# Kernel tuning notes

Hardware: AMD Instinct MI355X
Metric: run time of the kernel (lower is better)

Reference implementation:

```python
import jax, jax.numpy as jnp
import numpy as np

D_MODEL = 1024
NUM_HEADS = 16
D_HEAD = D_MODEL // NUM_HEADS


def setup_inputs() -> dict:
    key = jax.random.key(0)
    ks = jax.random.split(key, 10)
    B, L = 2, 2048
    s = 1.0 / np.sqrt(D_MODEL)
    inp = {
        'x_q': jax.random.normal(ks[0], (B, L, D_MODEL), jnp.float32),
        'x_kv': jax.random.normal(ks[1], (B, L, D_MODEL), jnp.float32),
        'wq': jax.random.normal(ks[2], (D_MODEL, D_MODEL), jnp.float32) * s,
        'bq': jnp.zeros((D_MODEL,), jnp.float32),
        'wk': jax.random.normal(ks[3], (D_MODEL, D_MODEL), jnp.float32) * s,
        'bk': jnp.zeros((D_MODEL,), jnp.float32),
        'wv': jax.random.normal(ks[4], (D_MODEL, D_MODEL), jnp.float32) * s,
        'bv': jnp.zeros((D_MODEL,), jnp.float32),
        'wo': jax.random.normal(ks[5], (D_MODEL, D_MODEL), jnp.float32) * s,
        'bo': jnp.zeros((D_MODEL,), jnp.float32),
    }
    return inp


def _split_heads(x):
    B, L, _ = x.shape
    return x.reshape(B, L, NUM_HEADS, D_HEAD).transpose(0, 2, 1, 3)  # (B,H,L,Dh)


def reference(x_q, x_kv, wq, bq, wk, bk, wv, bv, wo, bo):
    # Linear projections (torch Linear: x @ W^T + b)
    q = _split_heads(x_q @ wq.T + bq)   # (B,H,Lq,Dh)
    k = _split_heads(x_kv @ wk.T + bk)  # (B,H,Lk,Dh)
    v = _split_heads(x_kv @ wv.T + bv)  # (B,H,Lk,Dh)
    scale = 1.0 / jnp.sqrt(jnp.asarray(D_HEAD, q.dtype))
    scores = jnp.einsum('bhqd,bhkd->bhqk', q, k) * scale
    attn = jax.nn.softmax(scores, axis=-1)
    out = jnp.einsum('bhqk,bhkd->bhqd', attn, v)  # (B,H,Lq,Dh)
    B, H, Lq, Dh = out.shape
    out = out.transpose(0, 2, 1, 3).reshape(B, Lq, H * Dh)
    # dropout is identity in eval mode
    return out @ wo.T + bo
```

## Files before the change

kernel.cpp:

```cpp
#include <hip/hip_runtime.h>
#include <hip/hip_bf16.h>

typedef _Float16 __attribute__((ext_vector_type(8))) half8;
typedef _Float16 __attribute__((ext_vector_type(4))) half4;
typedef __fp16 __attribute__((ext_vector_type(2))) fp16x2;
typedef __fp16 __attribute__((ext_vector_type(4))) fp16x4;
typedef float __attribute__((ext_vector_type(4))) f32x4;

typedef __attribute__((address_space(1))) void gvoid_t;
typedef __attribute__((address_space(3))) void lvoid_t;

__device__ __forceinline__ void gld_lds16(const void* g, void* l) {
    __builtin_amdgcn_global_load_lds((const gvoid_t*)g, (lvoid_t*)l, 16, 0, 0);
}

__global__ void cvt_all(const float* __restrict__ x_q, const float* __restrict__ x_kv,
                        const float* __restrict__ wq, const float* __restrict__ wk,
                        const float* __restrict__ wv, const float* __restrict__ wo,
                        _Float16* __restrict__ xq16, _Float16* __restrict__ xkv16,
                        _Float16* __restrict__ wq16, _Float16* __restrict__ wk16,
                        _Float16* __restrict__ wv16, _Float16* __restrict__ wo16)
{
    const int y = blockIdx.y;
    const int n = (y < 2) ? (4096 * 1024) : (1024 * 1024);
    int i = (blockIdx.x * 256 + threadIdx.x) * 8;
    if (i >= n) return;
    const float* in = (y == 0) ? x_q : (y == 1) ? x_kv : (y == 2) ? wq : (y == 3) ? wk : (y == 4) ? wv : wo;
    _Float16* out = (y == 0) ? xq16 : (y == 1) ? xkv16 : (y == 2) ? wq16 : (y == 3) ? wk16 : (y == 4) ? wv16 : wo16;
    float4 a = *(const float4*)(in + i);
    float4 b = *(const float4*)(in + i + 4);
    half8 h;
    h[0] = (_Float16)a.x; h[1] = (_Float16)a.y; h[2] = (_Float16)a.z; h[3] = (_Float16)a.w;
    h[4] = (_Float16)b.x; h[5] = (_Float16)b.y; h[6] = (_Float16)b.z; h[7] = (_Float16)b.w;
    *(half8*)(out + i) = h;
}

template <typename OutT, bool VT>
__device__ __forceinline__ void gemm_store(
    OutT* __restrict__ C, int N, int row0, int col, float bb, float osc, const f32x4& acc)
{
    if (VT) {
        int b = row0 >> 11, l0 = row0 & 2047, h = col >> 6, dh = col & 63;
        half4 hv;
#pragma unroll
        for (int r = 0; r < 4; ++r) hv[r] = (_Float16)((acc[r] + bb) * osc);
        *(half4*)&C[(size_t)(((b * 16 + h) * 64 + dh)) * 2048 + l0] = hv;
    } else {
#pragma unroll
        for (int r = 0; r < 4; ++r) {
            float v = (acc[r] + bb) * osc;
            C[(size_t)(row0 + r) * N + col] = (OutT)v;
        }
    }
}

template <typename OutT, bool VT>
__device__ __forceinline__ void gemm_body(
    const _Float16* __restrict__ A,
    const _Float16* __restrict__ W,
    const float* __restrict__ bias,
    OutT* __restrict__ C,
    int N, int K, int bm, int bn, float osc,
    _Float16* As, _Float16* Bs)
{
    const int tid = threadIdx.x;
    const int wv = tid >> 6;
    const int lane = tid & 63;
    const int lr = lane & 15;
    const int lk = lane >> 4;
    const int wm = wv >> 1, wn = wv & 1;

    auto stage = [&](int cb, int k0) {
#pragma unroll
        for (int i = 0; i < 2; ++i) {
            int chunk = i * 256 + tid;
            int row = chunk >> 3, c8 = chunk & 7;
            gld_lds16(A + (size_t)(bm * 64 + row) * K + k0 + c8 * 8, &As[cb * 4096 + chunk * 8]);
        }
#pragma unroll
        for (int i = 0; i < 4; ++i) {
            int chunk = i * 256 + tid;
            int row = chunk >> 3, c8 = chunk & 7;
            gld_lds16(W + (size_t)(bn * 128 + row) * K + k0 + c8 * 8, &Bs[cb * 8192 + chunk * 8]);
        }
    };

    f32x4 acc[2][4] = {};

    stage(0, 0);
    __syncthreads();

    for (int k2 = 0; k2 < K; k2 += 128) {
#pragma unroll
        for (int hf = 0; hf < 2; ++hf) {
            const int k0 = k2 + hf * 64;
            if (k0 + 64 < K) stage(hf ^ 1, k0 + 64);
#pragma unroll
            for (int kk = 0; kk < 2; ++kk) {
                half8 a[2], b[4];
#pragma unroll
                for (int m = 0; m < 2; ++m)
                    a[m] = *(const half8*)&As[hf * 4096 + (wm * 32 + m * 16 + lr) * 64 + kk * 32 + lk * 8];
#pragma unroll
                for (int n = 0; n < 4; ++n)
                    b[n] = *(const half8*)&Bs[hf * 8192 + (wn * 64 + n * 16 + lr) * 64 + kk * 32 + lk * 8];
#pragma unroll
                for (int m = 0; m < 2; ++m)
#pragma unroll
                    for (int n = 0; n < 4; ++n)
                        acc[m][n] = __builtin_amdgcn_mfma_f32_16x16x32_f16(a[m], b[n], acc[m][n], 0, 0, 0);
            }
            __syncthreads();
        }
    }

#pragma unroll
    for (int m = 0; m < 2; ++m)
#pragma unroll
        for (int n = 0; n < 4; ++n) {
            int row0 = bm * 64 + wm * 32 + m * 16 + lk * 4;
            int col  = bn * 128 + wn * 64 + n * 16 + lr;
            gemm_store<OutT, VT>(C, N, row0, col, bias[col], osc, acc[m][n]);
        }
}

__device__ __forceinline__ int xcd_swz512(int x) { return ((x & 7) << 6) | (x >> 3); }

template <typename OutT>
__global__ __launch_bounds__(256) void gemm_bt(
    const _Float16* __restrict__ A, const _Float16* __restrict__ W,
    const float* __restrict__ bias, OutT* __restrict__ C,
    int M, int N, int K)
{
    __shared__ _Float16 As[2 * 64 * 64];
    __shared__ _Float16 Bs[2 * 128 * 64];
    const int nbn = N >> 7;
    const int bid = xcd_swz512(blockIdx.x);
    gemm_body<OutT, false>(A, W, bias, C, N, K, bid / nbn, bid % nbn, 1.0f, As, Bs);
}

__global__ __launch_bounds__(256) void gemm_qkv(
    const _Float16* __restrict__ xq, const _Float16* __restrict__ xkv,
    const _Float16* __restrict__ wqp, const _Float16* __restrict__ wkp, const _Float16* __restrict__ wvp,
    const float* __restrict__ bq, const float* __restrict__ bk, const float* __restrict__ bvv,
    _Float16* __restrict__ Qb, _Float16* __restrict__ Kb, _Float16* __restrict__ VbT)
{
    __shared__ _Float16 As[2 * 64 * 64];
    __shared__ _Float16 Bs[2 * 128 * 64];
    const int z = blockIdx.y;
    const _Float16* A = (z == 0) ? xq : xkv;
    const _Float16* W = (z == 0) ? wqp : (z == 1) ? wkp : wvp;
    const float* bias = (z == 0) ? bq : (z == 1) ? bk : bvv;
    const int bid = xcd_swz512(blockIdx.x);
    const int bm = bid >> 3, bn = bid & 7;
    if (z == 2)
        gemm_body<_Float16, true>(A, W, bias, VbT, 1024, 1024, bm, bn, 1.0f, As, Bs);
    else
        gemm_body<_Float16, false>(A, W, bias, (z == 0) ? Qb : Kb, 1024, 1024, bm, bn,
                                   (z == 0) ? (0.125f * 1.44269504088896f) : 1.0f, As, Bs);
}

__global__ __launch_bounds__(256, 4) void attn_fwd(
    const _Float16* __restrict__ Q,
    const _Float16* __restrict__ Kt,
    const _Float16* __restrict__ VT,
    _Float16* __restrict__ O)
{
    constexpr int KT = 64;
    __shared__ __align__(16) _Float16 Ks[2][KT * 64];
    __shared__ __align__(16) _Float16 Vs[2][64 * KT];

    const int tid = threadIdx.x;
    const int wv = tid >> 6;
    const int lane = tid & 63;
    const int lr = lane & 15;
    const int lk = lane >> 4;
    const int id = ((blockIdx.x & 7) << 7) | (blockIdx.x >> 3);
    const int qb = id & 31;
    const int bh = id >> 5;
    const size_t base = (size_t)(bh >> 4) * (2048 * 1024) + (size_t)(bh & 15) * 64;
    const size_t vtbase = (size_t)bh * (64 * 2048);

    half8 qf[2];
    {
        const _Float16* qp = Q + base + (size_t)(qb * 64 + wv * 16 + lr) * 1024 + lk * 8;
        qf[0] = *(const half8*)qp;
        qf[1] = *(const half8*)(qp + 32);
    }

    auto stage = [&](int cb, int kt) {
#pragma unroll
        for (int i = 0; i < 2; ++i) {
            int chunk = i * 256 + tid;
            int row = chunk >> 3, c8 = chunk & 7;
            int c8s = c8 ^ (row & 7);
            gld_lds16(Kt + base + (size_t)(kt + row) * 1024 + c8s * 8, &Ks[cb][chunk * 8]);
        }
#pragma unroll
        for (int i = 0; i < 2; ++i) {
            int chunk = i * 256 + tid;
            int row = chunk >> 3, c8 = chunk & 7;
            int c8s = c8 ^ (row & 7);
            gld_lds16(VT + vtbase + (size_t)row * 2048 + kt + c8s * 8, &Vs[cb][chunk * 8]);
        }
    };

    half8 ones8;
#pragma unroll
    for (int j = 0; j < 8; ++j) ones8[j] = (_Float16)1.0f;

    f32x4 o[4] = {};
    f32x4 lsacc = {};

    stage(0, 0);
    __syncthreads();

    for (int kt2 = 0; kt2 < 2048; kt2 += 2 * KT) {
#pragma unroll
        for (int hf = 0; hf < 2; ++hf) {
            const int kt = kt2 + hf * KT;
            if (kt + KT < 2048) stage(hf ^ 1, kt + KT);

            const _Float16* kb0 = &Ks[hf][lr * 64 + ((lk     ^ (lr & 7)) << 3)];
            const _Float16* kb1 = &Ks[hf][lr * 64 + (((4|lk) ^ (lr & 7)) << 3)];

            f32x4 s[4] = {};
            __builtin_amdgcn_s_setprio(1);
#pragma unroll
            for (int n = 0; n < 4; ++n) {
                half8 a0 = *(const half8*)(kb0 + n * 1024);
                s[n] = __builtin_amdgcn_mfma_f32_16x16x32_f16(a0, qf[0], s[n], 0, 0, 0);
            }
#pragma unroll
            for (int n = 0; n < 4; ++n) {
                half8 a1 = *(const half8*)(kb1 + n * 1024);
                s[n] = __builtin_amdgcn_mfma_f32_16x16x32_f16(a1, qf[1], s[n], 0, 0, 0);
            }
            __builtin_amdgcn_s_setprio(0);

            half4 pf[4];
#pragma unroll
            for (int n = 0; n < 4; ++n) {
                float p0 = __builtin_amdgcn_exp2f(s[n][0]);
                float p1 = __builtin_amdgcn_exp2f(s[n][1]);
                float p2 = __builtin_amdgcn_exp2f(s[n][2]);
                float p3 = __builtin_amdgcn_exp2f(s[n][3]);
                fp16x2 lo = __builtin_amdgcn_cvt_pkrtz(p0, p1);
                fp16x2 hi = __builtin_amdgcn_cvt_pkrtz(p2, p3);
                fp16x4 pv4 = __builtin_shufflevector(lo, hi, 0, 1, 2, 3);
                pf[n] = __builtin_bit_cast(half4, pv4);
            }

            __builtin_amdgcn_s_setprio(1);
#pragma unroll
            for (int c = 0; c < 2; ++c) {
                half8 pp = __builtin_shufflevector(pf[2 * c], pf[2 * c + 1], 0, 1, 2, 3, 4, 5, 6, 7);
                lsacc = __builtin_amdgcn_mfma_f32_16x16x32_f16(ones8, pp, lsacc, 0, 0, 0);
#pragma unroll
                for (int nd = 0; nd < 4; ++nd) {
                    int drow = nd * 16 + lr;
                    int c8a = (4 * c)     + (lk >> 1);
                    int c8b = (4 * c + 2) + (lk >> 1);
                    half4 va0 = *(const half4*)&Vs[hf][drow * 64 + ((c8a ^ (drow & 7)) << 3) + ((lk & 1) << 2)];
                    half4 va1 = *(const half4*)&Vs[hf][drow * 64 + ((c8b ^ (drow & 7)) << 3) + ((lk & 1) << 2)];
                    half8 va = __builtin_shufflevector(va0, va1, 0, 1, 2, 3, 4, 5, 6, 7);
                    o[nd] = __builtin_amdgcn_mfma_f32_16x16x32_f16(va, pp, o[nd], 0, 0, 0);
                }
            }
            __builtin_amdgcn_s_setprio(0);

            __syncthreads();
        }
    }

    const float inv = 1.0f / lsacc[0];
    const size_t orow = base + (size_t)(qb * 64 + wv * 16 + lr) * 1024;
#pragma unroll
    for (int nd = 0; nd < 4; ++nd) {
        half4 hv;
#pragma unroll
        for (int r = 0; r < 4; ++r) hv[r] = (_Float16)(o[nd][r] * inv);
        *(half4*)&O[orow + nd * 16 + lk * 4] = hv;
    }
}

extern "C" void kernel_launch(void* const* d_in, const int* in_sizes, int n_in,
                              void* d_out, int out_size, void* d_ws, size_t ws_size,
                              hipStream_t stream) {
    const float* x_q  = (const float*)d_in[0];
    const float* x_kv = (const float*)d_in[1];
    const float* wq   = (const float*)d_in[2];
    const float* bq   = (const float*)d_in[3];
    const float* wk   = (const float*)d_in[4];
    const float* bk   = (const float*)d_in[5];
    const float* wvp  = (const float*)d_in[6];
    const float* bv   = (const float*)d_in[7];
    const float* wo   = (const float*)d_in[8];
    const float* bo   = (const float*)d_in[9];
    float* out = (float*)d_out;

    const size_t MX = (size_t)4096 * 1024;
    const size_t WX = (size_t)1024 * 1024;
    _Float16* ws    = (_Float16*)d_ws;
    _Float16* xq16  = ws;
    _Float16* xkv16 = xq16 + MX;
    _Float16* wq16  = xkv16 + MX;
    _Float16* wk16  = wq16 + WX;
    _Float16* wv16  = wk16 + WX;
    _Float16* wo16  = wv16 + WX;
    _Float16* Qb    = wo16 + WX;
    _Float16* Kb    = Qb + MX;
    _Float16* VbT   = Kb + MX;
    _Float16* AO    = VbT + MX;

    cvt_all<<<dim3(2048, 6), 256, 0, stream>>>(x_q, x_kv, wq, wk, wvp, wo,
                                               xq16, xkv16, wq16, wk16, wv16, wo16);

    gemm_qkv<<<dim3(512, 3), 256, 0, stream>>>(xq16, xkv16, wq16, wk16, wv16,
                                               bq, bk, bv, Qb, Kb, VbT);

    attn_fwd<<<dim3(1024), 256, 0, stream>>>(Qb, Kb, VbT, AO);

    gemm_bt<float><<<dim3(512), 256, 0, stream>>>(AO, wo16, bo, out, 4096, 1024, 1024);
}
```

Baseline: 134.8 us.

## Triple-buffer K/V tiles in attention with one barrier per tile

Moves the attention kernel's K/V shared-memory staging from double to triple buffering. It prefetches two tiles ahead and uses partial vmcnt waits plus a single barrier per tile, instead of a full wait and barrier after each compute. The goal is to hide global-to-LDS load latency and cut synchronisation stalls. In exchange, LDS use rises by half and launch bounds drop from 4 to 3 blocks per CU, which lowers occupancy.

```diff
diff --git a/kernel.cpp b/kernel.cpp
--- a/kernel.cpp
+++ b/kernel.cpp
@@ -160,15 +160,16 @@
                                    (z == 0) ? (0.125f * 1.44269504088896f) : 1.0f, As, Bs);
 }
 
-__global__ __launch_bounds__(256, 4) void attn_fwd(
+__global__ __launch_bounds__(256, 3) void attn_fwd(
     const _Float16* __restrict__ Q,
     const _Float16* __restrict__ Kt,
     const _Float16* __restrict__ VT,
     _Float16* __restrict__ O)
 {
     constexpr int KT = 64;
-    __shared__ __align__(16) _Float16 Ks[2][KT * 64];
-    __shared__ __align__(16) _Float16 Vs[2][64 * KT];
+    constexpr int NT = 2048 / KT;
+    __shared__ __align__(16) _Float16 Ks[3][KT * 64];
+    __shared__ __align__(16) _Float16 Vs[3][64 * KT];
 
     const int tid = threadIdx.x;
     const int wv = tid >> 6;
@@ -212,66 +213,75 @@
     f32x4 o[4] = {};
     f32x4 lsacc = {};
 
+    auto compute = [&](int cb) {
+        const _Float16* kb0 = &Ks[cb][lr * 64 + ((lk     ^ (lr & 7)) << 3)];
+        const _Float16* kb1 = &Ks[cb][lr * 64 + (((4|lk) ^ (lr & 7)) << 3)];
+
+        f32x4 s[4] = {};
+        __builtin_amdgcn_s_setprio(1);
+#pragma unroll
+        for (int n = 0; n < 4; ++n) {
+            half8 a0 = *(const half8*)(kb0 + n * 1024);
+            s[n] = __builtin_amdgcn_mfma_f32_16x16x32_f16(a0, qf[0], s[n], 0, 0, 0);
+        }
+#pragma unroll
+        for (int n = 0; n < 4; ++n) {
+            half8 a1 = *(const half8*)(kb1 + n * 1024);
+            s[n] = __builtin_amdgcn_mfma_f32_16x16x32_f16(a1, qf[1], s[n], 0, 0, 0);
+        }
+        __builtin_amdgcn_s_setprio(0);
+
+        half4 pf[4];
+#pragma unroll
+        for (int n = 0; n < 4; ++n) {
+            float p0 = __builtin_amdgcn_exp2f(s[n][0]);
+            float p1 = __builtin_amdgcn_exp2f(s[n][1]);
+            float p2 = __builtin_amdgcn_exp2f(s[n][2]);
+            float p3 = __builtin_amdgcn_exp2f(s[n][3]);
+            fp16x2 lo = __builtin_amdgcn_cvt_pkrtz(p0, p1);
+            fp16x2 hi = __builtin_amdgcn_cvt_pkrtz(p2, p3);
+            fp16x4 pv4 = __builtin_shufflevector(lo, hi, 0, 1, 2, 3);
+            pf[n] = __builtin_bit_cast(half4, pv4);
+        }
+
+        __builtin_amdgcn_s_setprio(1);
+#pragma unroll
+        for (int c = 0; c < 2; ++c) {
+            half8 pp = __builtin_shufflevector(pf[2 * c], pf[2 * c + 1], 0, 1, 2, 3, 4, 5, 6, 7);
+            lsacc = __builtin_amdgcn_mfma_f32_16x16x32_f16(ones8, pp, lsacc, 0, 0, 0);
+#pragma unroll
+            for (int nd = 0; nd < 4; ++nd) {
+                int drow = nd * 16 + lr;
+                int c8a = (4 * c)     + (lk >> 1);
+                int c8b = (4 * c + 2) + (lk >> 1);
+                half4 va0 = *(const half4*)&Vs[cb][drow * 64 + ((c8a ^ (drow & 7)) << 3) + ((lk & 1) << 2)];
+                half4 va1 = *(const half4*)&Vs[cb][drow * 64 + ((c8b ^ (drow & 7)) << 3) + ((lk & 1) << 2)];
+                half8 va = __builtin_shufflevector(va0, va1, 0, 1, 2, 3, 4, 5, 6, 7);
+                o[nd] = __builtin_amdgcn_mfma_f32_16x16x32_f16(va, pp, o[nd], 0, 0, 0);
+            }
+        }
+        __builtin_amdgcn_s_setprio(0);
+    };
+
     stage(0, 0);
-    __syncthreads();
-
-    for (int kt2 = 0; kt2 < 2048; kt2 += 2 * KT) {
-#pragma unroll
-        for (int hf = 0; hf < 2; ++hf) {
-            const int kt = kt2 + hf * KT;
-            if (kt + KT < 2048) stage(hf ^ 1, kt + KT);
-
-            const _Float16* kb0 = &Ks[hf][lr * 64 + ((lk     ^ (lr & 7)) << 3)];
-            const _Float16* kb1 = &Ks[hf][lr * 64 + (((4|lk) ^ (lr & 7)) << 3)];
-
-            f32x4 s[4] = {};
-            __builtin_amdgcn_s_setprio(1);
-#pragma unroll
-            for (int n = 0; n < 4; ++n) {
-                half8 a0 = *(const half8*)(kb0 + n * 1024);
-                s[n] = __builtin_amdgcn_mfma_f32_16x16x32_f16(a0, qf[0], s[n], 0, 0, 0);
-            }
-#pragma unroll
-            for (int n = 0; n < 4; ++n) {
-                half8 a1 = *(const half8*)(kb1 + n * 1024);
-                s[n] = __builtin_amdgcn_mfma_f32_16x16x32_f16(a1, qf[1], s[n], 0, 0, 0);
-            }
-            __builtin_amdgcn_s_setprio(0);
-
-            half4 pf[4];
-#pragma unroll
-            for (int n = 0; n < 4; ++n) {
-                float p0 = __builtin_amdgcn_exp2f(s[n][0]);
-                float p1 = __builtin_amdgcn_exp2f(s[n][1]);
-                float p2 = __builtin_amdgcn_exp2f(s[n][2]);
-                float p3 = __builtin_amdgcn_exp2f(s[n][3]);
-                fp16x2 lo = __builtin_amdgcn_cvt_pkrtz(p0, p1);
-                fp16x2 hi = __builtin_amdgcn_cvt_pkrtz(p2, p3);
-                fp16x4 pv4 = __builtin_shufflevector(lo, hi, 0, 1, 2, 3);
-                pf[n] = __builtin_bit_cast(half4, pv4);
-            }
-
-            __builtin_amdgcn_s_setprio(1);
-#pragma unroll
-            for (int c = 0; c < 2; ++c) {
-                half8 pp = __builtin_shufflevector(pf[2 * c], pf[2 * c + 1], 0, 1, 2, 3, 4, 5, 6, 7);
-                lsacc = __builtin_amdgcn_mfma_f32_16x16x32_f16(ones8, pp, lsacc, 0, 0, 0);
-#pragma unroll
-                for (int nd = 0; nd < 4; ++nd) {
-                    int drow = nd * 16 + lr;
-                    int c8a = (4 * c)     + (lk >> 1);
-                    int c8b = (4 * c + 2) + (lk >> 1);
-                    half4 va0 = *(const half4*)&Vs[hf][drow * 64 + ((c8a ^ (drow & 7)) << 3) + ((lk & 1) << 2)];
-                    half4 va1 = *(const half4*)&Vs[hf][drow * 64 + ((c8b ^ (drow & 7)) << 3) + ((lk & 1) << 2)];
-                    half8 va = __builtin_shufflevector(va0, va1, 0, 1, 2, 3, 4, 5, 6, 7);
-                    o[nd] = __builtin_amdgcn_mfma_f32_16x16x32_f16(va, pp, o[nd], 0, 0, 0);
-                }
-            }
-            __builtin_amdgcn_s_setprio(0);
-
-            __syncthreads();
-        }
-    }
+    stage(1, KT);
+
+    int bufC = 0, bufS = 2;
+    for (int t = 0; t < NT - 1; ++t) {
+        asm volatile("s_waitcnt vmcnt(4)" ::: "memory");
+        __builtin_amdgcn_s_barrier();
+        asm volatile("" ::: "memory");
+        if (t + 2 < NT) {
+            stage(bufS, (t + 2) * KT);
+            bufS = (bufS == 2) ? 0 : bufS + 1;
+        }
+        compute(bufC);
+        bufC = (bufC == 2) ? 0 : bufC + 1;
+    }
+    asm volatile("s_waitcnt vmcnt(0)" ::: "memory");
+    __builtin_amdgcn_s_barrier();
+    asm volatile("" ::: "memory");
+    compute(bufC);
 
     const float inv = 1.0f / lsacc[0];
     const size_t orow = base + (size_t)(qb * 64 + wv * 16 + lr) * 1024;
```

New measurement: 150.8 us. 1.12x slower.
